# Kernel tuning notes

Hardware: AMD Instinct MI355X
Metric: run time of the kernel (lower is better)

The kernel has to match this reference:

```python
import jax, jax.numpy as jnp
import numpy as np

DIM = 1024
NUM_HEADS = 16
HEAD_DIM = DIM // NUM_HEADS  # 64; only used for the softmax scale


def setup_inputs() -> dict:
    key = jax.random.key(0)
    ks = jax.random.split(key, 9)
    s = 1.0 / np.sqrt(DIM)
    return {
        "x": jax.random.normal(ks[0], (2, 4096, DIM), dtype=jnp.float32),
        "Wq": jax.random.normal(ks[1], (DIM, DIM), dtype=jnp.float32) * s,
        "bq": jnp.zeros((DIM,), dtype=jnp.float32),
        "Wk": jax.random.normal(ks[2], (DIM, DIM), dtype=jnp.float32) * s,
        "bk": jnp.zeros((DIM,), dtype=jnp.float32),
        "Wv": jax.random.normal(ks[3], (DIM, DIM), dtype=jnp.float32) * s,
        "bv": jnp.zeros((DIM,), dtype=jnp.float32),
        "Wo": jax.random.normal(ks[4], (DIM, DIM), dtype=jnp.float32) * s,
        "bo": jnp.zeros((DIM,), dtype=jnp.float32),
    }


def reference(x, Wq, bq, Wk, bk, Wv, bv, Wo, bo):
    # Projections (nn.Linear equivalents)
    q = jnp.einsum("bsd,df->bsf", x, Wq) + bq
    k = jnp.einsum("bsd,df->bsf", x, Wk) + bk
    v = jnp.einsum("bsd,df->bsf", x, Wv) + bv
    # Full-dim attention (no head split); scale uses head_dim per original code.
    scale = 1.0 / np.sqrt(HEAD_DIM)
    scores = jnp.einsum("bqd,bkd->bqk", q, k) * scale  # [B, S, S]
    attn = jax.nn.softmax(scores, axis=-1)
    out = jnp.einsum("bqk,bkd->bqd", attn, v)
    return jnp.einsum("bsd,df->bsf", out, Wo) + bo
```

## Files before the change

kernel.cpp:

```cpp
#include <hip/hip_runtime.h>

typedef unsigned short u16;
using bf16x8  = __attribute__((ext_vector_type(8))) __bf16;
using floatx4 = __attribute__((ext_vector_type(4))) float;

__device__ __forceinline__ u16 f2bf(float f) {
  unsigned int u = __builtin_bit_cast(unsigned int, f);
  u += 0x7fffu + ((u >> 16) & 1u);
  return (u16)(u >> 16);
}

#define AS1(p) ((const __attribute__((address_space(1))) void*)(p))
#define AS3(p) ((__attribute__((address_space(3))) void*)(p))

#define GEMM_PROLOGUE_AT(bmv, bnv)                                           \
  __shared__ u16 As[128 * 32];                                               \
  __shared__ u16 Bs[128 * 32];                                               \
  const int tid  = threadIdx.x;                                              \
  const int wave = tid >> 6, lane = tid & 63;                                \
  const int wm = (wave >> 1) * 64, wn = (wave & 1) * 64;                     \
  const long bm = (bmv), bn = (bnv);                                         \
  floatx4 acc[4][4] = {};                                                    \
  const int srow = lane >> 2;                                                \
  const int scol = (lane & 3) * 8;                                           \
  const int c0 = wave * 2, c1 = c0 + 1;                                      \
  const int fr = lane & 15;                                                  \
  const int kq = (lane >> 4) * 8;                                            \
  const int oc = (lane >> 4) * 4;

#define GEMM_PROLOGUE() GEMM_PROLOGUE_AT((long)blockIdx.y * 128, (long)blockIdx.x * 128)

#define GEMM_STAGE(Ab, Bb, K, k0)                                            \
    __syncthreads();                                                         \
    __builtin_amdgcn_global_load_lds(AS1(Ab + (long)(c0*16 + srow)*K + k0 + scol), AS3(As + c0*512), 16, 0, 0); \
    __builtin_amdgcn_global_load_lds(AS1(Ab + (long)(c1*16 + srow)*K + k0 + scol), AS3(As + c1*512), 16, 0, 0); \
    __builtin_amdgcn_global_load_lds(AS1(Bb + (long)(c0*16 + srow)*K + k0 + scol), AS3(Bs + c0*512), 16, 0, 0); \
    __builtin_amdgcn_global_load_lds(AS1(Bb + (long)(c1*16 + srow)*K + k0 + scol), AS3(Bs + c1*512), 16, 0, 0); \
    __syncthreads();                                                         \
    bf16x8 af[4], bfv[4];                                                    \
    _Pragma("unroll")                                                        \
    for (int mi = 0; mi < 4; ++mi)                                           \
      af[mi] = *(const bf16x8*)(As + (wm + mi*16 + fr)*32 + kq);             \
    _Pragma("unroll")                                                        \
    for (int ni = 0; ni < 4; ++ni)                                           \
      bfv[ni] = *(const bf16x8*)(Bs + (wn + ni*16 + fr)*32 + kq);

#define GEMM_KSTEP(Ab, Bb, K, k0)                                            \
  {                                                                          \
    GEMM_STAGE(Ab, Bb, K, k0)                                                \
    _Pragma("unroll")                                                        \
    for (int mi = 0; mi < 4; ++mi)                                           \
      _Pragma("unroll")                                                      \
      for (int ni = 0; ni < 4; ++ni)                                         \
        acc[mi][ni] = __builtin_amdgcn_mfma_f32_16x16x32_bf16(af[mi], bfv[ni], acc[mi][ni], 0, 0, 0); \
  }

#define GEMM_KSTEP_SWAP(Ab, Bb, K, k0)                                       \
  {                                                                          \
    GEMM_STAGE(Ab, Bb, K, k0)                                                \
    _Pragma("unroll")                                                        \
    for (int mi = 0; mi < 4; ++mi)                                           \
      _Pragma("unroll")                                                      \
      for (int ni = 0; ni < 4; ++ni)                                         \
        acc[mi][ni] = __builtin_amdgcn_mfma_f32_16x16x32_bf16(bfv[ni], af[mi], acc[mi][ni], 0, 0, 0); \
  }

__global__ __launch_bounds__(256) void gemm_bt(
    const u16* __restrict__ A, const u16* __restrict__ Bt,
    float* __restrict__ Cout, const float* __restrict__ bias, int N, int K)
{
  GEMM_PROLOGUE();
  const u16* Ab = A + bm * K;
  const u16* Bb = Bt + bn * K;
  for (int k0 = 0; k0 < K; k0 += 32) GEMM_KSTEP_SWAP(Ab, Bb, K, k0);

#pragma unroll
  for (int mi = 0; mi < 4; ++mi) {
    long row = bm + wm + mi*16 + fr;
#pragma unroll
    for (int ni = 0; ni < 4; ++ni) {
      long colb = bn + wn + ni*16 + oc;
      float4 bv4 = *(const float4*)(bias + colb);
      float4 o;
      o.x = acc[mi][ni][0] + bv4.x;
      o.y = acc[mi][ni][1] + bv4.y;
      o.z = acc[mi][ni][2] + bv4.z;
      o.w = acc[mi][ni][3] + bv4.w;
      *(float4*)(Cout + row * N + colb) = o;
    }
  }
}

__global__ __launch_bounds__(256) void gemm_qk_exp(
    const u16* __restrict__ q, const u16* __restrict__ k,
    u16* __restrict__ probs, float* __restrict__ lpartT, float alpha)
{
  const int N = 4096, K = 1024;
  const int lin = blockIdx.x + (blockIdx.y << 5) + (blockIdx.z << 10);
  const int xcd = lin & 7, j = lin >> 3;
  const long b = xcd >> 2;
  const int band = (xcd & 3) * 8;
  const int t = j >> 6, w = j & 63;
  const int bx = t * 8 + (w & 7);
  const int by = band + (w >> 3);

  const u16* A  = q + b * 4096 * 1024;
  const u16* Bt = k + b * 4096 * 1024;
  u16* P = probs + b * 4096L * 4096;
  float* lp = lpartT + b * 4096 * 64;

  GEMM_PROLOGUE_AT((long)by * 128, (long)bx * 128);
  const u16* Ab = A + bm * K;
  const u16* Bb = Bt + bn * K;
  for (int k0 = 0; k0 < K; k0 += 32) GEMM_KSTEP_SWAP(Ab, Bb, K, k0);

  float rowsum[4] = {0.f, 0.f, 0.f, 0.f};
#pragma unroll
  for (int mi = 0; mi < 4; ++mi) {
    long row = bm + wm + mi*16 + fr;
#pragma unroll
    for (int ni = 0; ni < 4; ++ni) {
      long colb = bn + wn + ni*16 + oc;
      float e0 = __expf(acc[mi][ni][0] * alpha);
      float e1 = __expf(acc[mi][ni][1] * alpha);
      float e2 = __expf(acc[mi][ni][2] * alpha);
      float e3 = __expf(acc[mi][ni][3] * alpha);
      rowsum[mi] += (e0 + e1) + (e2 + e3);
      ushort4 o;
      o.x = f2bf(e0); o.y = f2bf(e1); o.z = f2bf(e2); o.w = f2bf(e3);
      *(ushort4*)(P + row * N + colb) = o;
    }
  }
  const long cg = bx * 2 + (wn >> 6);
#pragma unroll
  for (int mi = 0; mi < 4; ++mi) {
    float s = rowsum[mi];
    s += __shfl_xor(s, 16); s += __shfl_xor(s, 32);
    if (lane < 16)
      lp[(bm + wm + mi*16 + lane) * 64 + cg] = s;
  }
}

__global__ __launch_bounds__(256) void gemm_qkv(
    const u16* __restrict__ A, const u16* __restrict__ Bt,
    u16* __restrict__ qb, u16* __restrict__ kb, u16* __restrict__ vT,
    const float* __restrict__ bq, const float* __restrict__ bk,
    const float* __restrict__ bv)
{
  const int K = 1024;
  GEMM_PROLOGUE();
  const u16* Ab = A + bm * K;
  const u16* Bb = Bt + bn * K;

  if (bn < 2048) {
    for (int k0 = 0; k0 < K; k0 += 32) GEMM_KSTEP_SWAP(Ab, Bb, K, k0);
    u16* C = (bn < 1024) ? qb : kb;
    const float* bias = (bn < 1024) ? bq : bk;
#pragma unroll
    for (int mi = 0; mi < 4; ++mi) {
      long row = bm + wm + mi*16 + fr;
#pragma unroll
      for (int ni = 0; ni < 4; ++ni) {
        long colg = bn + wn + ni*16 + oc;
        long cc = colg & 1023;
        float4 bv4 = *(const float4*)(bias + cc);
        ushort4 o;
        o.x = f2bf(acc[mi][ni][0] + bv4.x);
        o.y = f2bf(acc[mi][ni][1] + bv4.y);
        o.z = f2bf(acc[mi][ni][2] + bv4.z);
        o.w = f2bf(acc[mi][ni][3] + bv4.w);
        *(ushort4*)(C + row * 1024 + cc) = o;
      }
    }
  } else {
    for (int k0 = 0; k0 < K; k0 += 32) GEMM_KSTEP(Ab, Bb, K, k0);
    const int orow = (lane >> 4) * 4;
    const int ocol = lane & 15;
#pragma unroll
    for (int ni = 0; ni < 4; ++ni) {
      long col = bn + wn + ni*16 + ocol;
      float bvv = bv[col - 2048];
#pragma unroll
      for (int mi = 0; mi < 4; ++mi) {
        long row = bm + wm + mi*16 + orow;
        long b_ = row >> 12, s = row & 4095, d = col - 2048;
        ushort4 o;
        o.x = f2bf(acc[mi][ni][0] + bvv);
        o.y = f2bf(acc[mi][ni][1] + bvv);
        o.z = f2bf(acc[mi][ni][2] + bvv);
        o.w = f2bf(acc[mi][ni][3] + bvv);
        *(ushort4*)(vT + b_ * (1024L * 4096) + d * 4096L + s) = o;
      }
    }
  }
}

__global__ __launch_bounds__(256) void gemm_pv_splitk(
    const u16* __restrict__ probs, const u16* __restrict__ vT,
    float* __restrict__ pA, float* __restrict__ pB)
{
  const int N = 1024, K = 4096, Ks = 2048;
  const int lin = blockIdx.x + (blockIdx.y << 3) + (blockIdx.z << 8);
  const int xcd = lin & 7, j = lin >> 3;
  const int slice = xcd >> 1, half = xcd & 1;
  const long b = slice >> 1;
  const int sp = slice & 1;
  const int bx = j & 7;
  const int by = (j >> 3) * 2 + half;

  const u16* A  = probs + b * 4096L * 4096;
  const u16* Bt = vT + b * 1024L * 4096;
  float* part = (b ? pB : pA) + sp * 4096L * 1024;

  GEMM_PROLOGUE_AT((long)by * 128, (long)bx * 128);
  const u16* Ab = A + bm * K;
  const u16* Bb = Bt + bn * K;
  const int kbeg = sp * Ks, kend = kbeg + Ks;
  for (int k0 = kbeg; k0 < kend; k0 += 32) GEMM_KSTEP_SWAP(Ab, Bb, K, k0);

#pragma unroll
  for (int mi = 0; mi < 4; ++mi) {
    long row = bm + wm + mi*16 + fr;
#pragma unroll
    for (int ni = 0; ni < 4; ++ni) {
      long colb = bn + wn + ni*16 + oc;
      float4 o;
      o.x = acc[mi][ni][0]; o.y = acc[mi][ni][1];
      o.z = acc[mi][ni][2]; o.w = acc[mi][ni][3];
      *(float4*)(part + row * N + colb) = o;
    }
  }
}

__global__ __launch_bounds__(256) void reduce2_div_row(
    const float* __restrict__ pA, const float* __restrict__ pB,
    const float* __restrict__ lpartT, u16* __restrict__ ob)
{
  const int row = blockIdx.x;
  const long b = blockIdx.y;
  const int tid = threadIdx.x;
  const float* part = b ? pB : pA;
  const float* lp = lpartT + b * 4096 * 64;
  __shared__ float sl;
  if (tid < 64) {
    float s = lp[(long)row * 64 + tid];
#pragma unroll
    for (int off = 32; off; off >>= 1) s += __shfl_down(s, off);
    if (tid == 0) sl = s;
  }
  __syncthreads();
  const float inv = 1.0f / sl;
  const long base = (long)row * 1024 + tid * 4;
  float4 a  = *(const float4*)(part + base);
  float4 b2 = *(const float4*)(part + 4096L * 1024 + base);
  ushort4 o;
  o.x = f2bf((a.x + b2.x) * inv);
  o.y = f2bf((a.y + b2.y) * inv);
  o.z = f2bf((a.z + b2.z) * inv);
  o.w = f2bf((a.w + b2.w) * inv);
  *(ushort4*)(ob + b * 4096L * 1024 + base) = o;
}

__global__ __launch_bounds__(256) void cast_f32_to_bf16(
    const float* __restrict__ in, u16* __restrict__ out, int n4)
{
  int i = blockIdx.x * 256 + threadIdx.x;
  if (i >= n4) return;
  float4 f = ((const float4*)in)[i];
  ushort4 o;
  o.x = f2bf(f.x); o.y = f2bf(f.y); o.z = f2bf(f.z); o.w = f2bf(f.w);
  ((ushort4*)out)[i] = o;
}

__global__ void transpose_w4(
    const float* __restrict__ W0, const float* __restrict__ W1,
    const float* __restrict__ W2, const float* __restrict__ W3,
    u16* __restrict__ O0, u16* __restrict__ O1,
    u16* __restrict__ O2, u16* __restrict__ O3)
{
  __shared__ float tile[32][33];
  const int z = blockIdx.z;
  const float* in = (z == 0) ? W0 : (z == 1) ? W1 : (z == 2) ? W2 : W3;
  u16* out = (z == 0) ? O0 : (z == 1) ? O1 : (z == 2) ? O2 : O3;
  int bx = blockIdx.x * 32, by = blockIdx.y * 32;
  int tx = threadIdx.x, ty = threadIdx.y;
  for (int i = ty; i < 32; i += 8)
    tile[i][tx] = in[(long)(by + i) * 1024 + bx + tx];
  __syncthreads();
  for (int i = ty; i < 32; i += 8)
    out[(long)(bx + i) * 1024 + by + tx] = f2bf(tile[tx][i]);
}

extern "C" void kernel_launch(void* const* d_in, const int* in_sizes, int n_in,
                              void* d_out, int out_size, void* d_ws, size_t ws_size,
                              hipStream_t stream) {
  const float* x  = (const float*)d_in[0];
  const float* Wq = (const float*)d_in[1];
  const float* bq = (const float*)d_in[2];
  const float* Wk = (const float*)d_in[3];
  const float* bk = (const float*)d_in[4];
  const float* Wv = (const float*)d_in[5];
  const float* bv = (const float*)d_in[6];
  const float* Wo = (const float*)d_in[7];
  const float* bo = (const float*)d_in[8];
  float* out = (float*)d_out;

  const int B = 2, S = 4096, D = 1024;
  const long MS = (long)B * S;
  const long MB = 1L << 20;

  char* w = (char*)d_ws;
  u16* qb  = (u16*)(w);
  u16* kb  = (u16*)(w + 16 * MB);
  u16* vT  = (u16*)(w + 32 * MB);
  u16* xb  = (u16*)(w + 48 * MB);
  u16* ob  = xb;
  u16* WqkvT = (u16*)(w + 64 * MB);
  u16* WoT = WqkvT + 3072L * 1024;
  u16* probs = (u16*)(w + 72 * MB);
  float* partA = (float*)(w);
  float* partB = (float*)(w + 136 * MB);
  float* lpartT = (float*)d_out;

  cast_f32_to_bf16<<<dim3((unsigned)(MS * D / 4 / 256)), dim3(256), 0, stream>>>(
      x, xb, (int)(MS * D / 4));

  transpose_w4<<<dim3(32, 32, 4), dim3(32, 8), 0, stream>>>(
      Wq, Wk, Wv, Wo, WqkvT, WqkvT + 1024L * 1024, WqkvT + 2048L * 1024, WoT);

  gemm_qkv<<<dim3(3 * D / 128, MS / 128), 256, 0, stream>>>(
      xb, WqkvT, qb, kb, vT, bq, bk, bv);

  const float scale = 0.125f;
  gemm_qk_exp<<<dim3(S / 128, S / 128, B), 256, 0, stream>>>(
      qb, kb, probs, lpartT, scale);
  gemm_pv_splitk<<<dim3(D / 128, S / 128, 2 * B), 256, 0, stream>>>(
      probs, vT, partA, partB);
  reduce2_div_row<<<dim3(S, B), 256, 0, stream>>>(partA, partB, lpartT, ob);

  gemm_bt<<<dim3(D / 128, MS / 128), 256, 0, stream>>>(ob, WoT, out, bo, D, D);
}
```

Measured before the change: 427.1 us.

## Split PV GEMM four ways with bf16 partials and fuse prep kernels

```diff
diff --git a/kernel.cpp b/kernel.cpp
--- a/kernel.cpp
+++ b/kernel.cpp
@@ -8,6 +8,10 @@
   unsigned int u = __builtin_bit_cast(unsigned int, f);
   u += 0x7fffu + ((u >> 16) & 1u);
   return (u16)(u >> 16);
+}
+__device__ __forceinline__ float bf2f(u16 h) {
+  unsigned int u = ((unsigned int)h) << 16;
+  return __builtin_bit_cast(float, u);
 }
 
 #define AS1(p) ((const __attribute__((address_space(1))) void*)(p))
@@ -197,20 +201,19 @@
 
 __global__ __launch_bounds__(256) void gemm_pv_splitk(
     const u16* __restrict__ probs, const u16* __restrict__ vT,
-    float* __restrict__ pA, float* __restrict__ pB)
-{
-  const int N = 1024, K = 4096, Ks = 2048;
+    u16* __restrict__ pA, u16* __restrict__ pB)
+{
+  const int N = 1024, K = 4096, Ks = 1024;
   const int lin = blockIdx.x + (blockIdx.y << 3) + (blockIdx.z << 8);
   const int xcd = lin & 7, j = lin >> 3;
-  const int slice = xcd >> 1, half = xcd & 1;
-  const long b = slice >> 1;
-  const int sp = slice & 1;
+  const long b = xcd >> 2;
+  const int sp = xcd & 3;
   const int bx = j & 7;
-  const int by = (j >> 3) * 2 + half;
+  const int by = j >> 3;
 
   const u16* A  = probs + b * 4096L * 4096;
   const u16* Bt = vT + b * 1024L * 4096;
-  float* part = (b ? pB : pA) + sp * 4096L * 1024;
+  u16* part = (b ? pB : pA) + (long)sp * 4096 * 1024;
 
   GEMM_PROLOGUE_AT((long)by * 128, (long)bx * 128);
   const u16* Ab = A + bm * K;
@@ -224,22 +227,24 @@
 #pragma unroll
     for (int ni = 0; ni < 4; ++ni) {
       long colb = bn + wn + ni*16 + oc;
-      float4 o;
-      o.x = acc[mi][ni][0]; o.y = acc[mi][ni][1];
-      o.z = acc[mi][ni][2]; o.w = acc[mi][ni][3];
-      *(float4*)(part + row * N + colb) = o;
-    }
-  }
-}
-
-__global__ __launch_bounds__(256) void reduce2_div_row(
-    const float* __restrict__ pA, const float* __restrict__ pB,
+      ushort4 o;
+      o.x = f2bf(acc[mi][ni][0]);
+      o.y = f2bf(acc[mi][ni][1]);
+      o.z = f2bf(acc[mi][ni][2]);
+      o.w = f2bf(acc[mi][ni][3]);
+      *(ushort4*)(part + row * N + colb) = o;
+    }
+  }
+}
+
+__global__ __launch_bounds__(256) void reduce4_div_row(
+    const u16* __restrict__ pA, const u16* __restrict__ pB,
     const float* __restrict__ lpartT, u16* __restrict__ ob)
 {
   const int row = blockIdx.x;
   const long b = blockIdx.y;
   const int tid = threadIdx.x;
-  const float* part = b ? pB : pA;
+  const u16* part = b ? pB : pA;
   const float* lp = lpartT + b * 4096 * 64;
   __shared__ float sl;
   if (tid < 64) {
@@ -251,44 +256,49 @@
   __syncthreads();
   const float inv = 1.0f / sl;
   const long base = (long)row * 1024 + tid * 4;
-  float4 a  = *(const float4*)(part + base);
-  float4 b2 = *(const float4*)(part + 4096L * 1024 + base);
+  float acc4[4] = {0.f, 0.f, 0.f, 0.f};
+#pragma unroll
+  for (int s = 0; s < 4; ++s) {
+    ushort4 p = *(const ushort4*)(part + (long)s * 4096 * 1024 + base);
+    acc4[0] += bf2f(p.x); acc4[1] += bf2f(p.y);
+    acc4[2] += bf2f(p.z); acc4[3] += bf2f(p.w);
+  }
   ushort4 o;
-  o.x = f2bf((a.x + b2.x) * inv);
-  o.y = f2bf((a.y + b2.y) * inv);
-  o.z = f2bf((a.z + b2.z) * inv);
-  o.w = f2bf((a.w + b2.w) * inv);
+  o.x = f2bf(acc4[0] * inv);
+  o.y = f2bf(acc4[1] * inv);
+  o.z = f2bf(acc4[2] * inv);
+  o.w = f2bf(acc4[3] * inv);
   *(ushort4*)(ob + b * 4096L * 1024 + base) = o;
 }
 
-__global__ __launch_bounds__(256) void cast_f32_to_bf16(
-    const float* __restrict__ in, u16* __restrict__ out, int n4)
-{
-  int i = blockIdx.x * 256 + threadIdx.x;
-  if (i >= n4) return;
-  float4 f = ((const float4*)in)[i];
-  ushort4 o;
-  o.x = f2bf(f.x); o.y = f2bf(f.y); o.z = f2bf(f.z); o.w = f2bf(f.w);
-  ((ushort4*)out)[i] = o;
-}
-
-__global__ void transpose_w4(
+__global__ __launch_bounds__(256) void prep(
+    const float* __restrict__ x, u16* __restrict__ xb,
     const float* __restrict__ W0, const float* __restrict__ W1,
     const float* __restrict__ W2, const float* __restrict__ W3,
     u16* __restrict__ O0, u16* __restrict__ O1,
     u16* __restrict__ O2, u16* __restrict__ O3)
 {
   __shared__ float tile[32][33];
-  const int z = blockIdx.z;
-  const float* in = (z == 0) ? W0 : (z == 1) ? W1 : (z == 2) ? W2 : W3;
-  u16* out = (z == 0) ? O0 : (z == 1) ? O1 : (z == 2) ? O2 : O3;
-  int bx = blockIdx.x * 32, by = blockIdx.y * 32;
-  int tx = threadIdx.x, ty = threadIdx.y;
-  for (int i = ty; i < 32; i += 8)
-    tile[i][tx] = in[(long)(by + i) * 1024 + bx + tx];
-  __syncthreads();
-  for (int i = ty; i < 32; i += 8)
-    out[(long)(bx + i) * 1024 + by + tx] = f2bf(tile[tx][i]);
+  int blk = blockIdx.x;
+  if (blk < 8192) {
+    int i = blk * 256 + threadIdx.x;
+    float4 f = ((const float4*)x)[i];
+    ushort4 o;
+    o.x = f2bf(f.x); o.y = f2bf(f.y); o.z = f2bf(f.z); o.w = f2bf(f.w);
+    ((ushort4*)xb)[i] = o;
+  } else {
+    blk -= 8192;
+    const int z = blk >> 10, t = blk & 1023;
+    const float* in = (z == 0) ? W0 : (z == 1) ? W1 : (z == 2) ? W2 : W3;
+    u16* outp = (z == 0) ? O0 : (z == 1) ? O1 : (z == 2) ? O2 : O3;
+    const int bx = (t & 31) * 32, by = (t >> 5) * 32;
+    const int tx = threadIdx.x & 31, ty = threadIdx.x >> 5;
+    for (int i = ty; i < 32; i += 8)
+      tile[i][tx] = in[(long)(by + i) * 1024 + bx + tx];
+    __syncthreads();
+    for (int i = ty; i < 32; i += 8)
+      outp[(long)(bx + i) * 1024 + by + tx] = f2bf(tile[tx][i]);
+  }
 }
 
 extern "C" void kernel_launch(void* const* d_in, const int* in_sizes, int n_in,
@@ -318,15 +328,13 @@
   u16* WqkvT = (u16*)(w + 64 * MB);
   u16* WoT = WqkvT + 3072L * 1024;
   u16* probs = (u16*)(w + 72 * MB);
-  float* partA = (float*)(w);
-  float* partB = (float*)(w + 136 * MB);
+  u16* partA = (u16*)(w);
+  u16* partB = (u16*)(w + 136 * MB);
   float* lpartT = (float*)d_out;
 
-  cast_f32_to_bf16<<<dim3((unsigned)(MS * D / 4 / 256)), dim3(256), 0, stream>>>(
-      x, xb, (int)(MS * D / 4));
-
-  transpose_w4<<<dim3(32, 32, 4), dim3(32, 8), 0, stream>>>(
-      Wq, Wk, Wv, Wo, WqkvT, WqkvT + 1024L * 1024, WqkvT + 2048L * 1024, WoT);
+  prep<<<dim3(8192 + 4096), 256, 0, stream>>>(
+      x, xb, Wq, Wk, Wv, Wo,
+      WqkvT, WqkvT + 1024L * 1024, WqkvT + 2048L * 1024, WoT);
 
   gemm_qkv<<<dim3(3 * D / 128, MS / 128), 256, 0, stream>>>(
       xb, WqkvT, qb, kb, vT, bq, bk, bv);
@@ -334,9 +342,9 @@
   const float scale = 0.125f;
   gemm_qk_exp<<<dim3(S / 128, S / 128, B), 256, 0, stream>>>(
       qb, kb, probs, lpartT, scale);
-  gemm_pv_splitk<<<dim3(D / 128, S / 128, 2 * B), 256, 0, stream>>>(
+  gemm_pv_splitk<<<dim3(D / 128, S / 128, 8), 256, 0, stream>>>(
       probs, vT, partA, partB);
-  reduce2_div_row<<<dim3(S, B), 256, 0, stream>>>(partA, partB, lpartT, ob);
+  reduce4_div_row<<<dim3(S, B), 256, 0, stream>>>(partA, partB, lpartT, ob);
 
   gemm_bt<<<dim3(D / 128, MS / 128), 256, 0, stream>>>(ob, WoT, out, bo, D, D);
 }
```

Result: faster. 409.2 us (-4.2%).
